# Performance work log

Measured on AMD Instinct MI355X. Metric: run time of the kernel, lower is better.

Reference implementation:

```python
import jax, jax.numpy as jnp
import numpy as np

IMG = 128          # image_size
TEX = 4            # texture_size (hard-coded in module)
WIDTH = float(np.tan(np.radians(30.0)))  # nr default viewing_angle=30
NEAR = 0.1
# images dict: values are [distance, azimuth, elevation]; eye = get_points_from_angles(dist, elev, azim)
VIEWS = [(2.83, 45.0, 0.0), (2.0, 0.0, 90.0), (3.46, 45.0, 45.0), (3.0, 0.0, 0.0)]  # (dist, elev, azim)


def _eye_from_angles(dist, elev_deg, azim_deg):
    e, a = np.radians(elev_deg), np.radians(azim_deg)
    return jnp.asarray([dist * np.cos(e) * np.sin(a), dist * np.sin(e), -dist * np.cos(e) * np.cos(a)], jnp.float32)


def _normalize(v):
    return v / jnp.linalg.norm(v)


def _trilinear(tex, c):
    # tex: [P, T, T, T, 3], c: [P, 3] continuous coords in [0, T-1]
    i0 = jnp.clip(jnp.floor(c).astype(jnp.int32), 0, TEX - 2)
    f = c - i0.astype(c.dtype)
    pi = jnp.arange(tex.shape[0])
    out = jnp.zeros((tex.shape[0], 3), tex.dtype)
    for dx in (0, 1):
        for dy in (0, 1):
            for dz in (0, 1):
                wgt = ((f[:, 0] if dx else 1.0 - f[:, 0])
                       * (f[:, 1] if dy else 1.0 - f[:, 1])
                       * (f[:, 2] if dz else 1.0 - f[:, 2]))
                out = out + wgt[:, None] * tex[pi, i0[:, 0] + dx, i0[:, 1] + dy, i0[:, 2] + dz]
    return out


def _render(verts, faces, tex, eye):
    # verts [V,3], faces [F,3] int, tex [F,T,T,T,3] -> image [1,3,IMG,IMG]
    # look_at transform (at=origin, up=+y)
    z_ax = _normalize(-eye)
    x_ax = _normalize(jnp.cross(jnp.asarray([0.0, 1.0, 0.0], jnp.float32), z_ax))
    y_ax = _normalize(jnp.cross(z_ax, x_ax))
    R = jnp.stack([x_ax, y_ax, z_ax])                       # [3,3]
    v = (verts - eye) @ R.T                                 # [V,3]
    # perspective projection
    z = v[:, 2]
    v = jnp.stack([v[:, 0] / (z * WIDTH), v[:, 1] / (z * WIDTH), z], -1)
    fv = v[faces]                                           # [F,3,3]

    # pixel grid in NDC [-1,1], row 0 = top
    s = (jnp.arange(IMG, dtype=jnp.float32) + 0.5) / IMG * 2.0 - 1.0
    px = jnp.broadcast_to(s[None, :], (IMG, IMG)).ravel()
    py = jnp.broadcast_to(-s[:, None], (IMG, IMG)).ravel()
    p = jnp.stack([px, py], -1)                             # [P,2]

    v0 = fv[:, 0, :2]
    e1 = fv[:, 1, :2] - v0
    e2 = fv[:, 2, :2] - v0
    det = e1[:, 0] * e2[:, 1] - e1[:, 1] * e2[:, 0]         # [F]
    ok = jnp.abs(det) > 1e-8
    inv_det = jnp.where(ok, 1.0 / jnp.where(ok, det, 1.0), 0.0)
    d = p[None, :, :] - v0[:, None, :]                      # [F,P,2]
    w1 = (e2[:, None, 1] * d[..., 0] - e2[:, None, 0] * d[..., 1]) * inv_det[:, None]
    w2 = (-e1[:, None, 1] * d[..., 0] + e1[:, None, 0] * d[..., 1]) * inv_det[:, None]
    w0 = 1.0 - w1 - w2
    fz = fv[:, :, 2]                                        # [F,3]
    depth = w0 * fz[:, 0:1] + w1 * fz[:, 1:2] + w2 * fz[:, 2:3]  # [F,P]
    visible = (w0 >= 0) & (w1 >= 0) & (w2 >= 0) & ok[:, None] & (depth > NEAR)
    depth_m = jnp.where(visible, depth, jnp.inf)
    fidx = jnp.argmin(depth_m, axis=0)                      # [P]
    P = fidx.shape[0]
    pi = jnp.arange(P)
    hit = jnp.isfinite(depth_m[fidx, pi])
    wsel = jnp.stack([w0[fidx, pi], w1[fidx, pi], w2[fidx, pi]], -1)  # [P,3]
    coords = jnp.clip(wsel, 0.0, 1.0) * (TEX - 1)
    color = _trilinear(tex[fidx], coords) * hit[:, None].astype(tex.dtype)  # [P,3]
    return color.reshape(IMG, IMG, 3).transpose(2, 0, 1)[None]  # [1,3,IMG,IMG]


def setup_inputs() -> dict:
    key = jax.random.key(0)
    k1, k2, k3, k4 = jax.random.split(key, 4)
    V, F = 1024, 1024
    vertices = jax.random.normal(k1, (1, V, 3), jnp.float32) * 0.5
    faces = jax.random.randint(k2, (1, F, 3), 0, V, jnp.int32)
    textures = jax.random.normal(k3, (1, F, TEX, TEX, TEX, 3), jnp.float32)
    image_refs = jax.random.uniform(k4, (4, 1, IMG, IMG), jnp.float32)
    return {"vertices": vertices, "faces": faces, "textures": textures, "image_refs": image_refs}


def reference(vertices, faces, textures, image_refs):
    tex = jnp.tanh(textures)[0]   # [F,T,T,T,3]
    verts = vertices[0]
    fcs = faces[0]
    loss = jnp.float32(0.0)
    for c, (dist, elev, azim) in enumerate(VIEWS):
        image = _render(verts, fcs, tex, _eye_from_angles(dist, elev, azim))  # [1,3,H,W]
        ref = image_refs[c][:, None]                                          # [1,1,H,W]
        loss = loss + jnp.sum((image - ref) ** 2)
    return loss
```

## Files before the change

kernel.cpp:

```cpp
#include <hip/hip_runtime.h>
#include <math.h>

#define IMG 128
#define NPIX (IMG * IMG)
#define NF 1024
#define NCHUNK 8
#define CHF 128
#define NEAR_Z 0.1f
#define NSHADE_BLK 256

struct AllViews { float m[4][12]; };

__device__ __forceinline__ void project_face(
    const float* __restrict__ verts, const int* __restrict__ faces,
    const float* M, float W, int f, float proj[3][3])
{
#pragma unroll
    for (int k = 0; k < 3; ++k) {
        int vi = faces[f * 3 + k];
        float px = verts[vi * 3 + 0] - M[9];
        float py = verts[vi * 3 + 1] - M[10];
        float pz = verts[vi * 3 + 2] - M[11];
        float x = M[0] * px + M[1] * py + M[2] * pz;
        float y = M[3] * px + M[4] * py + M[5] * pz;
        float z = M[6] * px + M[7] * py + M[8] * pz;
        proj[k][0] = x / (z * W);
        proj[k][1] = y / (z * W);
        proj[k][2] = z;
    }
}

__device__ __forceinline__ void face_planes(const float proj[3][3],
    float& a1x, float& a1y, float& b1, float& a2x, float& a2y, float& b2,
    float& ddx, float& ddy, float& dc)
{
    float v0x = proj[0][0], v0y = proj[0][1];
    float e1x = proj[1][0] - v0x, e1y = proj[1][1] - v0y;
    float e2x = proj[2][0] - v0x, e2y = proj[2][1] - v0y;
    float det = e1x * e2y - e1y * e2x;
    bool ok = fabsf(det) > 1e-8f;
    float inv = ok ? 1.0f / det : 0.0f;
    a1x = e2y * inv; a1y = -e2x * inv;
    b1 = -(a1x * v0x + a1y * v0y);
    a2x = -e1y * inv; a2y = e1x * inv;
    b2 = -(a2x * v0x + a2y * v0y);
    float g1 = proj[1][2] - proj[0][2];
    float g2 = proj[2][2] - proj[0][2];
    ddx = g1 * a1x + g2 * a2x;
    ddy = g1 * a1y + g2 * a2y;
    dc  = proj[0][2] + g1 * b1 + g2 * b2;
    if (!ok) dc = 0.0f;
}

__global__ __launch_bounds__(256) void raster(
    const float* __restrict__ verts, const int* __restrict__ faces,
    unsigned long long* __restrict__ keys, AllViews vc, float W)
{
    __shared__ float4 BB[CHF];
    __shared__ float4 P0[CHF];
    __shared__ float4 P1[CHF];
    __shared__ float  DC[CHF];

    int bid = blockIdx.x;
    int view  = bid >> 9;
    int b     = bid & 511;
    int chunk = b & (NCHUNK - 1);
    int ptile = b >> 3;
    int tid = threadIdx.x;

    if (tid < CHF) {
        int f = chunk * CHF + tid;
        float proj[3][3];
        project_face(verts, faces, vc.m[view], W, f, proj);
        float a1x, a1y, b1, a2x, a2y, b2, ddx, ddy, dc;
        face_planes(proj, a1x, a1y, b1, a2x, a2y, b2, ddx, ddy, dc);
        P0[tid] = make_float4(a1x, a1y, b1, a2x);
        P1[tid] = make_float4(a2y, b2, ddx, ddy);
        DC[tid] = dc;
        float ymin = fminf(fminf(proj[0][1], proj[1][1]), proj[2][1]);
        float ymax = fmaxf(fmaxf(proj[0][1], proj[1][1]), proj[2][1]);
        float xmin = fminf(fminf(proj[0][0], proj[1][0]), proj[2][0]);
        float xmax = fmaxf(fmaxf(proj[0][0], proj[1][0]), proj[2][0]);
        BB[tid] = make_float4(ymin, ymax, xmin, xmax);
    }
    __syncthreads();

    int p = ptile * 256 + tid;
    int row = p >> 7, col = p & 127;
    float sx = (col + 0.5f) * (2.0f / IMG) - 1.0f;
    float sy = -((row + 0.5f) * (2.0f / IMG) - 1.0f);
    int col0 = tid & 64;
    float wx0 = (col0 + 0.5f) * (2.0f / IMG) - 1.0f;
    float wx1 = (col0 + 63.5f) * (2.0f / IMG) - 1.0f;

    float best = INFINITY;
    int bf = 0;

    for (int f = 0; f < CHF; ++f) {
        float4 bb = BB[f];
        if (bb.x > sy || bb.y < sy || bb.z > wx1 || bb.w < wx0) continue;
        float4 Q0 = P0[f];
        float4 Q1 = P1[f];
        float dc  = DC[f];
        float w1  = fmaf(Q0.x, sx, fmaf(Q0.y, sy, Q0.z));
        float w2  = fmaf(Q0.w, sx, fmaf(Q1.x, sy, Q1.y));
        float dep = fmaf(Q1.z, sx, fmaf(Q1.w, sy, dc));
        bool vis  = (fminf(w1, w2) >= 0.0f) && (w1 + w2 <= 1.0f) && (dep > NEAR_Z);
        bool take = vis && (dep < best);
        best = take ? dep : best;
        bf   = take ? f : bf;
    }

    unsigned int dbits = __float_as_uint(best);
    unsigned long long key =
        ((unsigned long long)dbits << 32) | (unsigned int)(chunk * CHF + bf);
    keys[((size_t)(view * NCHUNK + chunk) << 14) + p] = key;
}

__global__ __launch_bounds__(256) void shade_loss(
    const float* __restrict__ verts, const int* __restrict__ faces,
    const unsigned long long* __restrict__ keys,
    const float* __restrict__ tex,
    const float* __restrict__ refs,
    float* __restrict__ partial, AllViews vc, float W)
{
    __shared__ float wsum[4];
    int t = blockIdx.x * blockDim.x + threadIdx.x;
    int view = t >> 14, p = t & (NPIX - 1);
    int row = p >> 7, col = p & 127;
    float sx = (col + 0.5f) * (2.0f / IMG) - 1.0f;
    float sy = -((row + 0.5f) * (2.0f / IMG) - 1.0f);

    const unsigned long long* kb = keys + ((size_t)(view * NCHUNK) << 14) + p;
    unsigned long long key = ~0ULL;
#pragma unroll
    for (int c = 0; c < NCHUNK; ++c) {
        unsigned long long k = kb[(size_t)c << 14];
        key = (k < key) ? k : key;
    }

    bool hit = (unsigned int)(key >> 32) < 0x7f800000u;
    float ref = refs[t];
    float lossv;
    if (hit) {
        int f = (int)(key & 0xffffffffu);
        float proj[3][3];
        project_face(verts, faces, vc.m[view], W, f, proj);
        float a1x, a1y, b1, a2x, a2y, b2, ddx, ddy, dc;
        face_planes(proj, a1x, a1y, b1, a2x, a2y, b2, ddx, ddy, dc);
        float w1 = fmaf(a1x, sx, fmaf(a1y, sy, b1));
        float w2 = fmaf(a2x, sx, fmaf(a2y, sy, b2));
        float w0 = 1.0f - w1 - w2;
        float cx = fminf(fmaxf(w0, 0.0f), 1.0f) * 3.0f;
        float cy = fminf(fmaxf(w1, 0.0f), 1.0f) * 3.0f;
        float cz = fminf(fmaxf(w2, 0.0f), 1.0f) * 3.0f;
        int ix = min(max((int)floorf(cx), 0), 2);
        int iy = min(max((int)floorf(cy), 0), 2);
        int iz = min(max((int)floorf(cz), 0), 2);
        float fx = cx - (float)ix, fy = cy - (float)iy, fz = cz - (float)iz;

        const float* T = tex + (size_t)f * 192;
        float c0 = 0.0f, c1 = 0.0f, c2 = 0.0f;
        for (int dxi = 0; dxi < 2; ++dxi)
            for (int dyi = 0; dyi < 2; ++dyi)
                for (int dzi = 0; dzi < 2; ++dzi) {
                    float w = (dxi ? fx : 1.0f - fx) *
                              (dyi ? fy : 1.0f - fy) *
                              (dzi ? fz : 1.0f - fz);
                    int base = (((ix + dxi) * 4 + (iy + dyi)) * 4 + (iz + dzi)) * 3;
                    c0 += w * tanhf(T[base + 0]);
                    c1 += w * tanhf(T[base + 1]);
                    c2 += w * tanhf(T[base + 2]);
                }
        float d0 = c0 - ref, d1 = c1 - ref, d2 = c2 - ref;
        lossv = d0 * d0 + d1 * d1 + d2 * d2;
    } else {
        lossv = 3.0f * ref * ref;
    }

    for (int off = 32; off; off >>= 1) lossv += __shfl_down(lossv, off);
    int tid = threadIdx.x;
    if ((tid & 63) == 0) wsum[tid >> 6] = lossv;
    __syncthreads();
    if (tid == 0) partial[blockIdx.x] = wsum[0] + wsum[1] + wsum[2] + wsum[3];
}

__global__ __launch_bounds__(256) void final_reduce(
    const float* __restrict__ partial, float* __restrict__ out)
{
    __shared__ float wsum[4];
    int tid = threadIdx.x;
    float v = partial[tid];
    for (int off = 32; off; off >>= 1) v += __shfl_down(v, off);
    if ((tid & 63) == 0) wsum[tid >> 6] = v;
    __syncthreads();
    if (tid == 0) out[0] = wsum[0] + wsum[1] + wsum[2] + wsum[3];
}

static void make_view(double dist, double elev, double azim, float* M)
{
    double e = elev * M_PI / 180.0, a = azim * M_PI / 180.0;
    float ex = (float)(dist * cos(e) * sin(a));
    float ey = (float)(dist * sin(e));
    float ez = (float)(-dist * cos(e) * cos(a));
    float zx = -ex, zy = -ey, zz = -ez;
    float n = sqrtf(zx * zx + zy * zy + zz * zz);
    zx /= n; zy /= n; zz /= n;
    float xx = zz, xy = 0.0f, xz = -zx;
    n = sqrtf(xx * xx + xy * xy + xz * xz);
    xx /= n; xy /= n; xz /= n;
    float yx = zy * xz - zz * xy;
    float yy = zz * xx - zx * xz;
    float yz = zx * xy - zy * xx;
    n = sqrtf(yx * yx + yy * yy + yz * yz);
    yx /= n; yy /= n; yz /= n;
    M[0] = xx; M[1] = xy; M[2] = xz;
    M[3] = yx; M[4] = yy; M[5] = yz;
    M[6] = zx; M[7] = zy; M[8] = zz;
    M[9] = ex; M[10] = ey; M[11] = ez;
}

extern "C" void kernel_launch(void* const* d_in, const int* in_sizes, int n_in,
                              void* d_out, int out_size, void* d_ws, size_t ws_size,
                              hipStream_t stream)
{
    const float* verts = (const float*)d_in[0];
    const int*   faces = (const int*)d_in[1];
    const float* tex   = (const float*)d_in[2];
    const float* refs  = (const float*)d_in[3];
    float* out = (float*)d_out;

    char* ws = (char*)d_ws;
    unsigned long long* keys = (unsigned long long*)ws;
    ws += (size_t)4 * NCHUNK * NPIX * sizeof(unsigned long long);
    float* partial = (float*)ws;

    AllViews vc;
    const double V[4][3] = {{2.83, 45.0, 0.0}, {2.0, 0.0, 90.0},
                            {3.46, 45.0, 45.0}, {3.0, 0.0, 0.0}};
    for (int i = 0; i < 4; ++i) make_view(V[i][0], V[i][1], V[i][2], vc.m[i]);
    float W = (float)tan(M_PI / 6.0);

    raster<<<2048, 256, 0, stream>>>(verts, faces, keys, vc, W);
    shade_loss<<<NSHADE_BLK, 256, 0, stream>>>(verts, faces, keys, tex, refs,
                                               partial, vc, W);
    final_reduce<<<1, 256, 0, stream>>>(partial, out);
}
```

Before: 46.67 us.

## Bin faces per row pair with ballot masks, 2x2 pixel blocking, fuse final reduce

Raster now builds per-row-pair ballot masks of faces whose y-extent overlaps, walks only set bits, and each thread evaluates a 2x2 pixel quad by incremental edge functions, quartering the block count. Depth is interpolated from barycentrics instead of precomputed plane coefficients. Shading uses an exp-based fast tanh with unrolled trilinear loops, and the final reduction is folded into the shade kernel via an atomic last-block counter, removing one launch. It risks precision differences from the fast tanh and relies on the counter reset done inside the raster kernel.

```diff
diff --git a/kernel.cpp b/kernel.cpp
--- a/kernel.cpp
+++ b/kernel.cpp
@@ -7,7 +7,7 @@
 #define NCHUNK 8
 #define CHF 128
 #define NEAR_Z 0.1f
-#define NSHADE_BLK 256
+#define DY 0.015625f
 
 struct AllViews { float m[4][12]; };
 
@@ -32,7 +32,7 @@
 
 __device__ __forceinline__ void face_planes(const float proj[3][3],
     float& a1x, float& a1y, float& b1, float& a2x, float& a2y, float& b2,
-    float& ddx, float& ddy, float& dc)
+    float& z0, float& g1, float& g2)
 {
     float v0x = proj[0][0], v0y = proj[0][1];
     float e1x = proj[1][0] - v0x, e1y = proj[1][1] - v0y;
@@ -44,77 +44,116 @@
     b1 = -(a1x * v0x + a1y * v0y);
     a2x = -e1y * inv; a2y = e1x * inv;
     b2 = -(a2x * v0x + a2y * v0y);
-    float g1 = proj[1][2] - proj[0][2];
-    float g2 = proj[2][2] - proj[0][2];
-    ddx = g1 * a1x + g2 * a2x;
-    ddy = g1 * a1y + g2 * a2y;
-    dc  = proj[0][2] + g1 * b1 + g2 * b2;
-    if (!ok) dc = 0.0f;
+    z0 = ok ? proj[0][2] : 0.0f;
+    g1 = proj[1][2] - proj[0][2];
+    g2 = proj[2][2] - proj[0][2];
+}
+
+__device__ __forceinline__ float fast_tanh(float x)
+{
+    float xc = fminf(fmaxf(x, -10.0f), 10.0f);
+    float e = __expf(2.0f * xc);
+    return __fdividef(e - 1.0f, e + 1.0f);
 }
 
 __global__ __launch_bounds__(256) void raster(
     const float* __restrict__ verts, const int* __restrict__ faces,
-    unsigned long long* __restrict__ keys, AllViews vc, float W)
-{
-    __shared__ float4 BB[CHF];
+    unsigned long long* __restrict__ keys, unsigned int* __restrict__ counter,
+    AllViews vc, float W)
+{
     __shared__ float4 P0[CHF];
     __shared__ float4 P1[CHF];
-    __shared__ float  DC[CHF];
+    __shared__ float  G2[CHF];
+    __shared__ unsigned long long MASK[4][2];
 
     int bid = blockIdx.x;
-    int view  = bid >> 9;
-    int b     = bid & 511;
+    int view  = bid >> 7;
+    int b     = bid & 127;
     int chunk = b & (NCHUNK - 1);
-    int ptile = b >> 3;
-    int tid = threadIdx.x;
-
+    int strip = b >> 3;
+    int tid  = threadIdx.x;
+    int wave = tid >> 6, lane = tid & 63;
+
+    if (bid == 0 && tid == 0) *counter = 0;
+
+    float ymin = INFINITY, ymax = -INFINITY;
     if (tid < CHF) {
         int f = chunk * CHF + tid;
         float proj[3][3];
         project_face(verts, faces, vc.m[view], W, f, proj);
-        float a1x, a1y, b1, a2x, a2y, b2, ddx, ddy, dc;
-        face_planes(proj, a1x, a1y, b1, a2x, a2y, b2, ddx, ddy, dc);
+        float a1x, a1y, b1, a2x, a2y, b2, z0, g1, g2;
+        face_planes(proj, a1x, a1y, b1, a2x, a2y, b2, z0, g1, g2);
         P0[tid] = make_float4(a1x, a1y, b1, a2x);
-        P1[tid] = make_float4(a2y, b2, ddx, ddy);
-        DC[tid] = dc;
-        float ymin = fminf(fminf(proj[0][1], proj[1][1]), proj[2][1]);
-        float ymax = fmaxf(fmaxf(proj[0][1], proj[1][1]), proj[2][1]);
-        float xmin = fminf(fminf(proj[0][0], proj[1][0]), proj[2][0]);
-        float xmax = fmaxf(fmaxf(proj[0][0], proj[1][0]), proj[2][0]);
-        BB[tid] = make_float4(ymin, ymax, xmin, xmax);
+        P1[tid] = make_float4(a2y, b2, z0, g1);
+        G2[tid] = g2;
+        if (z0 != 0.0f) {
+            ymin = fminf(fminf(proj[0][1], proj[1][1]), proj[2][1]);
+            ymax = fmaxf(fmaxf(proj[0][1], proj[1][1]), proj[2][1]);
+        }
+    }
+    if (wave < 2) {
+#pragma unroll
+        for (int rp = 0; rp < 4; ++rp) {
+            int r0 = strip * 8 + 2 * rp;
+            float syhi = 1.0f - (r0 + 0.5f) * DY;
+            float sylo = syhi - DY;
+            bool inter = (ymin <= syhi) && (ymax >= sylo);
+            unsigned long long m = __ballot(inter);
+            if (lane == 0) MASK[rp][wave] = m;
+        }
     }
     __syncthreads();
 
-    int p = ptile * 256 + tid;
-    int row = p >> 7, col = p & 127;
-    float sx = (col + 0.5f) * (2.0f / IMG) - 1.0f;
-    float sy = -((row + 0.5f) * (2.0f / IMG) - 1.0f);
-    int col0 = tid & 64;
-    float wx0 = (col0 + 0.5f) * (2.0f / IMG) - 1.0f;
-    float wx1 = (col0 + 63.5f) * (2.0f / IMG) - 1.0f;
-
-    float best = INFINITY;
-    int bf = 0;
-
-    for (int f = 0; f < CHF; ++f) {
-        float4 bb = BB[f];
-        if (bb.x > sy || bb.y < sy || bb.z > wx1 || bb.w < wx0) continue;
-        float4 Q0 = P0[f];
-        float4 Q1 = P1[f];
-        float dc  = DC[f];
-        float w1  = fmaf(Q0.x, sx, fmaf(Q0.y, sy, Q0.z));
-        float w2  = fmaf(Q0.w, sx, fmaf(Q1.x, sy, Q1.y));
-        float dep = fmaf(Q1.z, sx, fmaf(Q1.w, sy, dc));
-        bool vis  = (fminf(w1, w2) >= 0.0f) && (w1 + w2 <= 1.0f) && (dep > NEAR_Z);
-        bool take = vis && (dep < best);
-        best = take ? dep : best;
-        bf   = take ? f : bf;
-    }
-
-    unsigned int dbits = __float_as_uint(best);
-    unsigned long long key =
-        ((unsigned long long)dbits << 32) | (unsigned int)(chunk * CHF + bf);
-    keys[((size_t)(view * NCHUNK + chunk) << 14) + p] = key;
+    int r0 = strip * 8 + 2 * wave;
+    float sy0 = 1.0f - (r0 + 0.5f) * DY;
+    float sx0 = (lane + 0.5f) * DY - 1.0f;
+
+    float bst[4] = {INFINITY, INFINITY, INFINITY, INFINITY};
+    int   bfi[4] = {0, 0, 0, 0};
+
+#pragma unroll
+    for (int half = 0; half < 2; ++half) {
+        unsigned long long m = MASK[wave][half];
+        int fbase = half * 64;
+        while (m) {
+            int f = fbase + (int)__builtin_ctzll(m);
+            m &= m - 1;
+            float4 q0 = P0[f];
+            float4 q1 = P1[f];
+            float g2  = G2[f];
+            float w1_00 = fmaf(q0.x, sx0, fmaf(q0.y, sy0, q0.z));
+            float w2_00 = fmaf(q0.w, sx0, fmaf(q1.x, sy0, q1.y));
+            float w1_01 = w1_00 + q0.x;
+            float w2_01 = w2_00 + q0.w;
+            float w1_10 = fmaf(q0.y, -DY, w1_00);
+            float w2_10 = fmaf(q1.x, -DY, w2_00);
+            float w1_11 = w1_10 + q0.x;
+            float w2_11 = w2_10 + q0.w;
+            float w1q[4] = {w1_00, w1_01, w1_10, w1_11};
+            float w2q[4] = {w2_00, w2_01, w2_10, w2_11};
+#pragma unroll
+            for (int q = 0; q < 4; ++q) {
+                float w1 = w1q[q], w2 = w2q[q];
+                float dep = fmaf(w2, g2, fmaf(w1, q1.w, q1.z));
+                bool vis = (fminf(w1, w2) >= 0.0f) && (w1 + w2 <= 1.0f) &&
+                           (dep > NEAR_Z);
+                bool take = vis && (dep < bst[q]);
+                bst[q] = take ? dep : bst[q];
+                bfi[q] = take ? f : bfi[q];
+            }
+        }
+    }
+
+    size_t base = ((size_t)(view * NCHUNK + chunk) << 14);
+    int p00 = r0 * IMG + lane;
+    int fo = chunk * CHF;
+#pragma unroll
+    for (int q = 0; q < 4; ++q) {
+        unsigned long long key =
+            ((unsigned long long)__float_as_uint(bst[q]) << 32) |
+            (unsigned int)(fo + bfi[q]);
+        keys[base + p00 + (q & 1) * 64 + (q >> 1) * IMG] = key;
+    }
 }
 
 __global__ __launch_bounds__(256) void shade_loss(
@@ -122,14 +161,17 @@
     const unsigned long long* __restrict__ keys,
     const float* __restrict__ tex,
     const float* __restrict__ refs,
-    float* __restrict__ partial, AllViews vc, float W)
+    float* __restrict__ partial, unsigned int* __restrict__ counter,
+    float* __restrict__ out, AllViews vc, float W)
 {
     __shared__ float wsum[4];
-    int t = blockIdx.x * blockDim.x + threadIdx.x;
+    __shared__ bool last;
+    int tid = threadIdx.x;
+    int t = blockIdx.x * 256 + tid;
     int view = t >> 14, p = t & (NPIX - 1);
     int row = p >> 7, col = p & 127;
-    float sx = (col + 0.5f) * (2.0f / IMG) - 1.0f;
-    float sy = -((row + 0.5f) * (2.0f / IMG) - 1.0f);
+    float sx = (col + 0.5f) * DY - 1.0f;
+    float sy = 1.0f - (row + 0.5f) * DY;
 
     const unsigned long long* kb = keys + ((size_t)(view * NCHUNK) << 14) + p;
     unsigned long long key = ~0ULL;
@@ -146,8 +188,8 @@
         int f = (int)(key & 0xffffffffu);
         float proj[3][3];
         project_face(verts, faces, vc.m[view], W, f, proj);
-        float a1x, a1y, b1, a2x, a2y, b2, ddx, ddy, dc;
-        face_planes(proj, a1x, a1y, b1, a2x, a2y, b2, ddx, ddy, dc);
+        float a1x, a1y, b1, a2x, a2y, b2, z0, g1, g2;
+        face_planes(proj, a1x, a1y, b1, a2x, a2y, b2, z0, g1, g2);
         float w1 = fmaf(a1x, sx, fmaf(a1y, sy, b1));
         float w2 = fmaf(a2x, sx, fmaf(a2y, sy, b2));
         float w0 = 1.0f - w1 - w2;
@@ -161,16 +203,19 @@
 
         const float* T = tex + (size_t)f * 192;
         float c0 = 0.0f, c1 = 0.0f, c2 = 0.0f;
+#pragma unroll
         for (int dxi = 0; dxi < 2; ++dxi)
+#pragma unroll
             for (int dyi = 0; dyi < 2; ++dyi)
+#pragma unroll
                 for (int dzi = 0; dzi < 2; ++dzi) {
                     float w = (dxi ? fx : 1.0f - fx) *
                               (dyi ? fy : 1.0f - fy) *
                               (dzi ? fz : 1.0f - fz);
                     int base = (((ix + dxi) * 4 + (iy + dyi)) * 4 + (iz + dzi)) * 3;
-                    c0 += w * tanhf(T[base + 0]);
-                    c1 += w * tanhf(T[base + 1]);
-                    c2 += w * tanhf(T[base + 2]);
+                    c0 += w * fast_tanh(T[base + 0]);
+                    c1 += w * fast_tanh(T[base + 1]);
+                    c2 += w * fast_tanh(T[base + 2]);
                 }
         float d0 = c0 - ref, d1 = c1 - ref, d2 = c2 - ref;
         lossv = d0 * d0 + d1 * d1 + d2 * d2;
@@ -179,22 +224,23 @@
     }
 
     for (int off = 32; off; off >>= 1) lossv += __shfl_down(lossv, off);
-    int tid = threadIdx.x;
     if ((tid & 63) == 0) wsum[tid >> 6] = lossv;
     __syncthreads();
-    if (tid == 0) partial[blockIdx.x] = wsum[0] + wsum[1] + wsum[2] + wsum[3];
-}
-
-__global__ __launch_bounds__(256) void final_reduce(
-    const float* __restrict__ partial, float* __restrict__ out)
-{
-    __shared__ float wsum[4];
-    int tid = threadIdx.x;
-    float v = partial[tid];
-    for (int off = 32; off; off >>= 1) v += __shfl_down(v, off);
-    if ((tid & 63) == 0) wsum[tid >> 6] = v;
+    if (tid == 0) {
+        partial[blockIdx.x] = wsum[0] + wsum[1] + wsum[2] + wsum[3];
+        __threadfence();
+        unsigned int old = atomicAdd(counter, 1);
+        last = (old == (unsigned int)(gridDim.x - 1));
+    }
     __syncthreads();
-    if (tid == 0) out[0] = wsum[0] + wsum[1] + wsum[2] + wsum[3];
+    if (last) {
+        __threadfence();
+        float v = partial[tid];
+        for (int off = 32; off; off >>= 1) v += __shfl_down(v, off);
+        if ((tid & 63) == 0) wsum[tid >> 6] = v;
+        __syncthreads();
+        if (tid == 0) out[0] = wsum[0] + wsum[1] + wsum[2] + wsum[3];
+    }
 }
 
 static void make_view(double dist, double elev, double azim, float* M)
@@ -234,6 +280,8 @@
     unsigned long long* keys = (unsigned long long*)ws;
     ws += (size_t)4 * NCHUNK * NPIX * sizeof(unsigned long long);
     float* partial = (float*)ws;
+    ws += 256 * sizeof(float);
+    unsigned int* counter = (unsigned int*)ws;
 
     AllViews vc;
     const double V[4][3] = {{2.83, 45.0, 0.0}, {2.0, 0.0, 90.0},
@@ -241,8 +289,7 @@
     for (int i = 0; i < 4; ++i) make_view(V[i][0], V[i][1], V[i][2], vc.m[i]);
     float W = (float)tan(M_PI / 6.0);
 
-    raster<<<2048, 256, 0, stream>>>(verts, faces, keys, vc, W);
-    shade_loss<<<NSHADE_BLK, 256, 0, stream>>>(verts, faces, keys, tex, refs,
-                                               partial, vc, W);
-    final_reduce<<<1, 256, 0, stream>>>(partial, out);
-}
+    raster<<<512, 256, 0, stream>>>(verts, faces, keys, counter, vc, W);
+    shade_loss<<<256, 256, 0, stream>>>(verts, faces, keys, tex, refs,
+                                        partial, counter, out, vc, W);
+}
```

Result: faster. 44.39 us (-4.9%).
